# Kernel tuning notes

Hardware: AMD Instinct MI355X
Metric: run time of the kernel (lower is better)

The kernel has to match this reference:

```python
import jax, jax.numpy as jnp
import numpy as np

N_NODES = 50000


def _sage_conv(x, src, dst, Wl, bl, Wr):
    # mean-aggregate source features onto targets (PyG SAGEConv, aggr='mean')
    msg = x[src]                                             # [E, C_in] gather
    s = jax.ops.segment_sum(msg, dst, num_segments=N_NODES)  # [N, C_in]
    cnt = jax.ops.segment_sum(jnp.ones((src.shape[0],), x.dtype), dst,
                              num_segments=N_NODES)          # [N]
    agg = s / jnp.maximum(cnt, 1.0)[:, None]
    # out = lin_l(agg) + lin_r(x); bias only on lin_l
    return agg @ Wl.T + bl + x @ Wr.T


def setup_inputs() -> dict:
    key = jax.random.key(0)
    ks = jax.random.split(key, 8)
    in_c, hid_c, out_c = 128, 128, 64
    n_edges = 800000
    x = jax.random.normal(ks[0], (N_NODES, in_c), dtype=jnp.float32)
    edge_index = jax.random.randint(ks[1], (2, n_edges), 0, N_NODES, dtype=jnp.int64)
    sc = lambda k, shp: jax.random.normal(k, shp, dtype=jnp.float32) / np.sqrt(shp[1])
    return {
        "x": x,
        "edge_index": edge_index,
        "W1l": sc(ks[2], (hid_c, in_c)),
        "b1l": jnp.zeros((hid_c,), jnp.float32),
        "W1r": sc(ks[3], (hid_c, in_c)),
        "W2l": sc(ks[4], (out_c, hid_c)),
        "b2l": jnp.zeros((out_c,), jnp.float32),
        "W2r": sc(ks[5], (out_c, hid_c)),
    }


def reference(x, edge_index, W1l, b1l, W1r, W2l, b2l, W2r):
    src, dst = edge_index[0], edge_index[1]
    h = jax.nn.relu(_sage_conv(x, src, dst, W1l, b1l, W1r))
    # dropout(p=0.5) is identity at inference (training=False)
    return _sage_conv(h, src, dst, W2l, b2l, W2r)
```

## Files before the change

kernel.cpp:

```cpp
#include <hip/hip_runtime.h>
#include <hip/hip_bf16.h>

#define N_NODES 50000
#define N_EDGES 800000
#define N_BUCKETS 196
#define BUCKET_CAP 8192
#define POISON 0xAAAAAAAAu

#define XCVT_BLK 6250
#define WCVT_BLK 48
#define EPB 2048
#define BKT_BLK 391

typedef __attribute__((ext_vector_type(8))) short short8;
typedef __attribute__((ext_vector_type(4))) float floatx4;

static __device__ __forceinline__ float bf16_lo(unsigned int v) {
  union { unsigned int u; float f; } c; c.u = v << 16; return c.f;
}
static __device__ __forceinline__ float bf16_hi(unsigned int v) {
  union { unsigned int u; float f; } c; c.u = v & 0xffff0000u; return c.f;
}
static __device__ __forceinline__ unsigned short f32_to_bf16_rne(float f) {
  union { float f; unsigned int u; } c; c.f = f;
  unsigned int u = c.u;
  unsigned int r = (u + 0x7fffu + ((u >> 16) & 1u)) >> 16;
  return (unsigned short)r;
}
static __device__ __forceinline__ unsigned int pack2(float a, float b) {
  return (unsigned int)f32_to_bf16_rne(a) | ((unsigned int)f32_to_bf16_rne(b) << 16);
}
static __device__ __forceinline__ uint2 pack4(float4 v) {
  return (uint2){pack2(v.x, v.y), pack2(v.z, v.w)};
}
static __device__ __forceinline__ void accum8(float* acc, uint4 v) {
  acc[0] += bf16_lo(v.x); acc[1] += bf16_hi(v.x);
  acc[2] += bf16_lo(v.y); acc[3] += bf16_hi(v.y);
  acc[4] += bf16_lo(v.z); acc[5] += bf16_hi(v.z);
  acc[6] += bf16_lo(v.w); acc[7] += bf16_hi(v.w);
}

__global__ __launch_bounds__(256) void prep_bucket_kernel(
    const float4* __restrict__ x4, uint2* __restrict__ xb4,
    const float4* __restrict__ w1l4, const float4* __restrict__ w1r4,
    const float4* __restrict__ w2l4, const float4* __restrict__ w2r4,
    uint2* __restrict__ o1l, uint2* __restrict__ o1r,
    uint2* __restrict__ o2l, uint2* __restrict__ o2r,
    const int* __restrict__ src, const int* __restrict__ dst,
    unsigned int* __restrict__ bcur, unsigned int* __restrict__ ebuf) {
  __shared__ int hist[N_BUCKETS];
  __shared__ int base[N_BUCKETS];
  const int b = blockIdx.x, tid = threadIdx.x;
  if (b < XCVT_BLK) {
    int i = b * 256 + tid;
    xb4[i] = pack4(x4[i]);
    return;
  }
  if (b < XCVT_BLK + WCVT_BLK) {
    int j = (b - XCVT_BLK) * 256 + tid;
    const float4* in; uint2* out; int o2, NJ;
    if (j < 4096)       { in = w1l4; out = o1l; o2 = j;         NJ = 128; }
    else if (j < 8192)  { in = w1r4; out = o1r; o2 = j - 4096;  NJ = 128; }
    else if (j < 10240) { in = w2l4; out = o2l; o2 = j - 8192;  NJ = 64; }
    else                { in = w2r4; out = o2r; o2 = j - 10240; NJ = 64; }
    int half = o2 & 1;
    int rest = o2 >> 1;
    int col  = rest % NJ;
    int qk   = rest / NJ;
    int quad = qk & 3, kb = qk >> 2;
    out[o2] = pack4(in[col * 32 + kb * 8 + quad * 2 + half]);
    return;
  }
  const int eb = b - XCVT_BLK - WCVT_BLK;
  for (int i = tid; i < N_BUCKETS; i += 256) hist[i] = 0;
  __syncthreads();
  const int e0 = eb * EPB;
  int bk[8], rk[8];
  unsigned int pk[8];
  bool val[8];
  #pragma unroll
  for (int k = 0; k < 8; ++k) {
    int e = e0 + k * 256 + tid;
    val[k] = (e < N_EDGES);
    if (val[k]) {
      int d = dst[e], s = src[e];
      bk[k] = d >> 8;
      pk[k] = ((unsigned int)(d & 255) << 16) | (unsigned int)s;
      rk[k] = atomicAdd(&hist[bk[k]], 1);
    }
  }
  __syncthreads();
  for (int i = tid; i < N_BUCKETS; i += 256) {
    int h = hist[i];
    base[i] = h ? (int)(atomicAdd(&bcur[i], (unsigned int)h) - POISON) : 0;
  }
  __syncthreads();
  #pragma unroll
  for (int k = 0; k < 8; ++k) {
    if (val[k]) {
      unsigned int p = (unsigned int)(base[bk[k]] + rk[k]);
      if (p < BUCKET_CAP) ebuf[(size_t)bk[k] * BUCKET_CAP + p] = pk[k];
    }
  }
}

__global__ __launch_bounds__(256) void local_csr_kernel(
    const unsigned int* __restrict__ ebuf, const unsigned int* __restrict__ bcur,
    int* __restrict__ start_g, int* __restrict__ cnt_g, int* __restrict__ eidx) {
  const int b = blockIdx.x;
  int nb = (int)(bcur[b] - POISON);
  nb = max(0, min(nb, BUCKET_CAP));
  __shared__ int cnt[256];
  __shared__ int loff[256];
  __shared__ int ws[4];
  cnt[threadIdx.x] = 0;
  __syncthreads();
  const unsigned int* eb = ebuf + (size_t)b * BUCKET_CAP;
  for (int i = threadIdx.x; i < nb; i += 256)
    atomicAdd(&cnt[eb[i] >> 16], 1);
  __syncthreads();
  const int lane = threadIdx.x & 63, wid = threadIdx.x >> 6;
  int v = cnt[threadIdx.x];
  int incl = v;
  #pragma unroll
  for (int d = 1; d < 64; d <<= 1) {
    int t = __shfl_up(incl, d, 64);
    if (lane >= d) incl += t;
  }
  if (lane == 63) ws[wid] = incl;
  __syncthreads();
  int add = 0;
  #pragma unroll
  for (int w = 0; w < 4; ++w) if (w < wid) add += ws[w];
  int excl = add + incl - v;
  loff[threadIdx.x] = excl;
  int node = b * 256 + threadIdx.x;
  if (node < N_NODES) {
    start_g[node] = b * BUCKET_CAP + excl;
    cnt_g[node] = v;
  }
  __syncthreads();
  for (int i = threadIdx.x; i < nb; i += 256) {
    unsigned int p = eb[i];
    int pos = atomicAdd(&loff[p >> 16], 1);
    eidx[(size_t)b * BUCKET_CAP + pos] = (int)(p & 0xffffu);
  }
}

__global__ __launch_bounds__(256) void agg_kernel(
    const uint4* __restrict__ in,
    const int* __restrict__ start_g, const int* __restrict__ cnt_g,
    const int* __restrict__ eidx, uint4* __restrict__ out) {
  const int lane = threadIdx.x & 63;
  const int sub = lane >> 4;
  const int l16 = lane & 15;
  int node = blockIdx.x * 4 + (threadIdx.x >> 6);
  if (node >= N_NODES) return;
  int e0 = start_g[node];
  int c = cnt_g[node];
  int e1 = e0 + c;

  float acc[8];
  #pragma unroll
  for (int t = 0; t < 8; ++t) acc[t] = 0.f;

  int e = e0;
  for (; e + 16 <= e1; e += 16) {
    int s0 = eidx[e + sub];
    int s1 = eidx[e + 4 + sub];
    int s2 = eidx[e + 8 + sub];
    int s3 = eidx[e + 12 + sub];
    uint4 v0 = in[(size_t)s0 * 16 + l16];
    uint4 v1 = in[(size_t)s1 * 16 + l16];
    uint4 v2 = in[(size_t)s2 * 16 + l16];
    uint4 v3 = in[(size_t)s3 * 16 + l16];
    accum8(acc, v0); accum8(acc, v1); accum8(acc, v2); accum8(acc, v3);
  }
  for (; e + 8 <= e1; e += 8) {
    int s0 = eidx[e + sub];
    int s1 = eidx[e + 4 + sub];
    uint4 v0 = in[(size_t)s0 * 16 + l16];
    uint4 v1 = in[(size_t)s1 * 16 + l16];
    accum8(acc, v0); accum8(acc, v1);
  }
  for (; e < e1; e += 4) {
    int ee = e + sub;
    if (ee < e1) accum8(acc, in[(size_t)eidx[ee] * 16 + l16]);
  }
  #pragma unroll
  for (int d = 16; d < 64; d <<= 1) {
    #pragma unroll
    for (int t = 0; t < 8; ++t) acc[t] += __shfl_xor(acc[t], d, 64);
  }
  if (sub == 0) {
    float inv = 1.0f / fmaxf((float)c, 1.0f);
    uint4 o;
    o.x = pack2(acc[0] * inv, acc[1] * inv);
    o.y = pack2(acc[2] * inv, acc[3] * inv);
    o.z = pack2(acc[4] * inv, acc[5] * inv);
    o.w = pack2(acc[6] * inv, acc[7] * inv);
    out[(size_t)node * 16 + l16] = o;
  }
}

__global__ __launch_bounds__(256) void fused_gemm_kernel(
    const uint4* __restrict__ aggb4, const uint4* __restrict__ xb4,
    const unsigned short* __restrict__ W1l, const unsigned short* __restrict__ W1r,
    const float* __restrict__ b1,
    const unsigned short* __restrict__ W2l, const unsigned short* __restrict__ W2r,
    const float* __restrict__ b2,
    unsigned short* __restrict__ z, unsigned short* __restrict__ rbuf) {
  __shared__ unsigned short lds_a[64 * 136];
  __shared__ unsigned short lds_x[64 * 136];
  const int tid = threadIdx.x, lane = tid & 63, wave = tid >> 6;
  const int quad = lane >> 4, r16 = lane & 15;
  const int cg = wave & 1, tw = wave >> 1;
  const int col0 = cg * 64;
  const int n0 = blockIdx.x * 64;

  #pragma unroll
  for (int k = 0; k < 4; ++k) {
    int idx = k * 256 + tid;
    int row = idx >> 4, col = idx & 15;
    int gr = n0 + row; if (gr >= N_NODES) gr = N_NODES - 1;
    ((uint4*)lds_a)[row * 17 + col] = aggb4[(size_t)gr * 16 + col];
    ((uint4*)lds_x)[row * 17 + col] = xb4[(size_t)gr * 16 + col];
  }
  __syncthreads();

  const unsigned short* As[2] = {lds_a, lds_x};
  const unsigned short* Ws[2] = {W1l, W1r};
  floatx4 acc1[2][4] = {};
  #pragma unroll
  for (int rt = 0; rt < 2; ++rt) {
    int lrow = tw * 32 + rt * 16;
    #pragma unroll
    for (int s = 0; s < 2; ++s) {
      const unsigned short* Ar = As[s] + (lrow + r16) * 136 + quad * 8;
      #pragma unroll
      for (int kb = 0; kb < 4; ++kb) {
        short8 a = *(const short8*)(Ar + kb * 32);
        const unsigned short* Wf = Ws[s] + ((size_t)(kb * 4 + quad) * 128) * 8;
        #pragma unroll
        for (int c = 0; c < 4; ++c) {
          short8 bfr = *(const short8*)(Wf + (size_t)(col0 + c * 16 + r16) * 8);
          acc1[rt][c] = __builtin_amdgcn_mfma_f32_16x16x32_bf16(a, bfr, acc1[rt][c], 0, 0, 0);
        }
      }
    }
  }
  __syncthreads();

  #pragma unroll
  for (int rt = 0; rt < 2; ++rt) {
    int lrow0 = tw * 32 + rt * 16 + quad * 4;
    #pragma unroll
    for (int c = 0; c < 4; ++c) {
      int j = col0 + c * 16 + r16;
      float bv = b1[j];
      #pragma unroll
      for (int r = 0; r < 4; ++r)
        lds_a[(lrow0 + r) * 136 + j] = f32_to_bf16_rne(fmaxf(acc1[rt][c][r] + bv, 0.f));
    }
  }
  __syncthreads();

  const unsigned short* W = cg ? W2r : W2l;
  unsigned short* outp = cg ? rbuf : z;
  #pragma unroll
  for (int rt = 0; rt < 2; ++rt) {
    int lrow = tw * 32 + rt * 16;
    floatx4 acc[4] = {};
    const unsigned short* la = lds_a + (lrow + r16) * 136 + quad * 8;
    #pragma unroll
    for (int kb = 0; kb < 4; ++kb) {
      short8 a = *(const short8*)(la + kb * 32);
      const unsigned short* Wf = W + ((size_t)(kb * 4 + quad) * 64) * 8;
      #pragma unroll
      for (int c = 0; c < 4; ++c) {
        short8 bfr = *(const short8*)(Wf + (size_t)(c * 16 + r16) * 8);
        acc[c] = __builtin_amdgcn_mfma_f32_16x16x32_bf16(a, bfr, acc[c], 0, 0, 0);
      }
    }
    int orow0 = n0 + lrow + quad * 4;
    #pragma unroll
    for (int c = 0; c < 4; ++c) {
      int j = c * 16 + r16;
      float bv = cg ? b2[j] : 0.f;
      #pragma unroll
      for (int r = 0; r < 4; ++r) {
        int node = orow0 + r;
        if (node < N_NODES)
          outp[(size_t)node * 64 + j] = f32_to_bf16_rne(acc[c][r] + bv);
      }
    }
  }
}

__global__ __launch_bounds__(256) void final_agg_kernel(
    const uint4* __restrict__ z4, const uint4* __restrict__ r4,
    const int* __restrict__ start_g, const int* __restrict__ cnt_g,
    const int* __restrict__ eidx, float* __restrict__ outp) {
  const int lane = threadIdx.x & 63;
  const int sub = lane >> 3;
  const int l8 = lane & 7;
  int node = blockIdx.x * 4 + (threadIdx.x >> 6);
  if (node >= N_NODES) return;
  int e0 = start_g[node];
  int c = cnt_g[node];
  int e1 = e0 + c;

  float acc[8];
  #pragma unroll
  for (int t = 0; t < 8; ++t) acc[t] = 0.f;

  int e = e0;
  for (; e + 16 <= e1; e += 16) {
    int s0 = eidx[e + sub];
    int s1 = eidx[e + 8 + sub];
    uint4 v0 = z4[(size_t)s0 * 8 + l8];
    uint4 v1 = z4[(size_t)s1 * 8 + l8];
    accum8(acc, v0);
    accum8(acc, v1);
  }
  for (; e < e1; e += 8) {
    int ee = e + sub;
    if (ee < e1) accum8(acc, z4[(size_t)eidx[ee] * 8 + l8]);
  }
  #pragma unroll
  for (int d = 8; d < 64; d <<= 1) {
    #pragma unroll
    for (int t = 0; t < 8; ++t) acc[t] += __shfl_xor(acc[t], d, 64);
  }
  if (sub == 0) {
    float inv = 1.0f / fmaxf((float)c, 1.0f);
    uint4 rv = r4[(size_t)node * 8 + l8];
    float4* op = (float4*)(outp + (size_t)node * 64 + l8 * 8);
    float4 a, b;
    a.x = acc[0] * inv + bf16_lo(rv.x); a.y = acc[1] * inv + bf16_hi(rv.x);
    a.z = acc[2] * inv + bf16_lo(rv.y); a.w = acc[3] * inv + bf16_hi(rv.y);
    b.x = acc[4] * inv + bf16_lo(rv.z); b.y = acc[5] * inv + bf16_hi(rv.z);
    b.z = acc[6] * inv + bf16_lo(rv.w); b.w = acc[7] * inv + bf16_hi(rv.w);
    op[0] = a; op[1] = b;
  }
}

extern "C" void kernel_launch(void* const* d_in, const int* in_sizes, int n_in,
                              void* d_out, int out_size, void* d_ws, size_t ws_size,
                              hipStream_t stream) {
  (void)in_sizes; (void)n_in; (void)out_size; (void)ws_size;
  const float* x   = (const float*)d_in[0];
  const int*   ei  = (const int*)d_in[1];
  const float* W1l = (const float*)d_in[2];
  const float* b1l = (const float*)d_in[3];
  const float* W1r = (const float*)d_in[4];
  const float* W2l = (const float*)d_in[5];
  const float* b2l = (const float*)d_in[6];
  const float* W2r = (const float*)d_in[7];
  const int* src = ei;
  const int* dst = ei + N_EDGES;

  char* ws = (char*)d_ws;
  size_t p = 0;
  auto alloc = [&](size_t bytes) {
    char* q = ws + p;
    p = (p + bytes + 255) & ~(size_t)255;
    return q;
  };
  unsigned int* bcur = (unsigned int*)alloc((size_t)N_BUCKETS * 4);
  int* start_g = (int*)alloc((size_t)N_NODES * 4);
  int* cnt_g   = (int*)alloc((size_t)N_NODES * 4);
  unsigned int* ebuf = (unsigned int*)alloc((size_t)N_BUCKETS * BUCKET_CAP * 4);
  int* eidx    = (int*)alloc((size_t)N_BUCKETS * BUCKET_CAP * 4);
  unsigned short* xb   = (unsigned short*)alloc((size_t)N_NODES * 128 * 2);
  unsigned short* aggb = (unsigned short*)alloc((size_t)N_NODES * 128 * 2);
  unsigned short* zb   = (unsigned short*)alloc((size_t)N_NODES * 64 * 2);
  unsigned short* rb   = (unsigned short*)alloc((size_t)N_NODES * 64 * 2);
  unsigned short* w1lb = (unsigned short*)alloc(128 * 128 * 2);
  unsigned short* w1rb = (unsigned short*)alloc(128 * 128 * 2);
  unsigned short* w2lb = (unsigned short*)alloc(64 * 128 * 2);
  unsigned short* w2rb = (unsigned short*)alloc(64 * 128 * 2);

  prep_bucket_kernel<<<XCVT_BLK + WCVT_BLK + BKT_BLK, 256, 0, stream>>>(
      (const float4*)x, (uint2*)xb,
      (const float4*)W1l, (const float4*)W1r, (const float4*)W2l, (const float4*)W2r,
      (uint2*)w1lb, (uint2*)w1rb, (uint2*)w2lb, (uint2*)w2rb,
      src, dst, bcur, (unsigned int*)ebuf);
  local_csr_kernel<<<N_BUCKETS, 256, 0, stream>>>(
      (const unsigned int*)ebuf, bcur, start_g, cnt_g, eidx);
  agg_kernel<<<(N_NODES + 3) / 4, 256, 0, stream>>>(
      (const uint4*)xb, start_g, cnt_g, eidx, (uint4*)aggb);
  fused_gemm_kernel<<<(N_NODES + 63) / 64, 256, 0, stream>>>(
      (const uint4*)aggb, (const uint4*)xb, w1lb, w1rb, b1l, w2lb, w2rb, b2l, zb, rb);
  final_agg_kernel<<<(N_NODES + 3) / 4, 256, 0, stream>>>(
      (const uint4*)zb, (const uint4*)rb, start_g, cnt_g, eidx, (float*)d_out);
}
```

Baseline: 189.5 us.

## Map one small lane group per node in aggregation kernels and widen CSR block

Both aggregation kernels now give each node a 16-lane (or 8-lane) group instead of a full wave. Each group walks its edges serially with 8 gathers in flight per step, so the cross-lane shuffle reduction and the idle-lane masking on the final write go away, and more nodes share each wave. The local CSR build runs 512 threads per bucket, with only the first 256 doing the scan. The trade-off is less edge-level parallelism per node, so high-degree nodes may become a longer serial tail. The first aggregation kernel also drops its node bounds check, which is only safe because the node count divides evenly by 16.

```diff
diff --git a/kernel.cpp b/kernel.cpp
--- a/kernel.cpp
+++ b/kernel.cpp
@@ -104,7 +104,7 @@
   }
 }
 
-__global__ __launch_bounds__(256) void local_csr_kernel(
+__global__ __launch_bounds__(512) void local_csr_kernel(
     const unsigned int* __restrict__ ebuf, const unsigned int* __restrict__ bcur,
     int* __restrict__ start_g, int* __restrict__ cnt_g, int* __restrict__ eidx) {
   const int b = blockIdx.x;
@@ -113,34 +113,37 @@
   __shared__ int cnt[256];
   __shared__ int loff[256];
   __shared__ int ws[4];
-  cnt[threadIdx.x] = 0;
+  if (threadIdx.x < 256) cnt[threadIdx.x] = 0;
   __syncthreads();
   const unsigned int* eb = ebuf + (size_t)b * BUCKET_CAP;
-  for (int i = threadIdx.x; i < nb; i += 256)
+  for (int i = threadIdx.x; i < nb; i += 512)
     atomicAdd(&cnt[eb[i] >> 16], 1);
   __syncthreads();
-  const int lane = threadIdx.x & 63, wid = threadIdx.x >> 6;
-  int v = cnt[threadIdx.x];
+  const int t256 = threadIdx.x & 255;
+  const int lane = threadIdx.x & 63, wid = (threadIdx.x >> 6) & 3;
+  int v = cnt[t256];
   int incl = v;
   #pragma unroll
   for (int d = 1; d < 64; d <<= 1) {
     int t = __shfl_up(incl, d, 64);
     if (lane >= d) incl += t;
   }
-  if (lane == 63) ws[wid] = incl;
+  if (threadIdx.x < 256 && lane == 63) ws[wid] = incl;
   __syncthreads();
   int add = 0;
   #pragma unroll
   for (int w = 0; w < 4; ++w) if (w < wid) add += ws[w];
   int excl = add + incl - v;
-  loff[threadIdx.x] = excl;
-  int node = b * 256 + threadIdx.x;
-  if (node < N_NODES) {
-    start_g[node] = b * BUCKET_CAP + excl;
-    cnt_g[node] = v;
-  }
-  __syncthreads();
-  for (int i = threadIdx.x; i < nb; i += 256) {
+  if (threadIdx.x < 256) {
+    loff[t256] = excl;
+    int node = b * 256 + t256;
+    if (node < N_NODES) {
+      start_g[node] = b * BUCKET_CAP + excl;
+      cnt_g[node] = v;
+    }
+  }
+  __syncthreads();
+  for (int i = threadIdx.x; i < nb; i += 512) {
     unsigned int p = eb[i];
     int pos = atomicAdd(&loff[p >> 16], 1);
     eidx[(size_t)b * BUCKET_CAP + pos] = (int)(p & 0xffffu);
@@ -151,11 +154,8 @@
     const uint4* __restrict__ in,
     const int* __restrict__ start_g, const int* __restrict__ cnt_g,
     const int* __restrict__ eidx, uint4* __restrict__ out) {
-  const int lane = threadIdx.x & 63;
-  const int sub = lane >> 4;
-  const int l16 = lane & 15;
-  int node = blockIdx.x * 4 + (threadIdx.x >> 6);
-  if (node >= N_NODES) return;
+  const int l16 = threadIdx.x & 15;
+  const int node = blockIdx.x * 16 + (threadIdx.x >> 4);
   int e0 = start_g[node];
   int c = cnt_g[node];
   int e1 = e0 + c;
@@ -165,42 +165,37 @@
   for (int t = 0; t < 8; ++t) acc[t] = 0.f;
 
   int e = e0;
-  for (; e + 16 <= e1; e += 16) {
-    int s0 = eidx[e + sub];
-    int s1 = eidx[e + 4 + sub];
-    int s2 = eidx[e + 8 + sub];
-    int s3 = eidx[e + 12 + sub];
-    uint4 v0 = in[(size_t)s0 * 16 + l16];
-    uint4 v1 = in[(size_t)s1 * 16 + l16];
-    uint4 v2 = in[(size_t)s2 * 16 + l16];
-    uint4 v3 = in[(size_t)s3 * 16 + l16];
-    accum8(acc, v0); accum8(acc, v1); accum8(acc, v2); accum8(acc, v3);
-  }
   for (; e + 8 <= e1; e += 8) {
-    int s0 = eidx[e + sub];
-    int s1 = eidx[e + 4 + sub];
-    uint4 v0 = in[(size_t)s0 * 16 + l16];
-    uint4 v1 = in[(size_t)s1 * 16 + l16];
-    accum8(acc, v0); accum8(acc, v1);
-  }
-  for (; e < e1; e += 4) {
-    int ee = e + sub;
-    if (ee < e1) accum8(acc, in[(size_t)eidx[ee] * 16 + l16]);
-  }
-  #pragma unroll
-  for (int d = 16; d < 64; d <<= 1) {
-    #pragma unroll
-    for (int t = 0; t < 8; ++t) acc[t] += __shfl_xor(acc[t], d, 64);
-  }
-  if (sub == 0) {
-    float inv = 1.0f / fmaxf((float)c, 1.0f);
-    uint4 o;
-    o.x = pack2(acc[0] * inv, acc[1] * inv);
-    o.y = pack2(acc[2] * inv, acc[3] * inv);
-    o.z = pack2(acc[4] * inv, acc[5] * inv);
-    o.w = pack2(acc[6] * inv, acc[7] * inv);
-    out[(size_t)node * 16 + l16] = o;
-  }
+    int s[8];
+    #pragma unroll
+    for (int k = 0; k < 8; ++k) s[k] = eidx[e + k];
+    uint4 v[8];
+    #pragma unroll
+    for (int k = 0; k < 8; ++k) v[k] = in[(size_t)s[k] * 16 + l16];
+    #pragma unroll
+    for (int k = 0; k < 8; ++k) accum8(acc, v[k]);
+  }
+  if (e + 4 <= e1) {
+    int s[4];
+    #pragma unroll
+    for (int k = 0; k < 4; ++k) s[k] = eidx[e + k];
+    uint4 v[4];
+    #pragma unroll
+    for (int k = 0; k < 4; ++k) v[k] = in[(size_t)s[k] * 16 + l16];
+    #pragma unroll
+    for (int k = 0; k < 4; ++k) accum8(acc, v[k]);
+    e += 4;
+  }
+  for (; e < e1; ++e)
+    accum8(acc, in[(size_t)eidx[e] * 16 + l16]);
+
+  float inv = 1.0f / fmaxf((float)c, 1.0f);
+  uint4 o;
+  o.x = pack2(acc[0] * inv, acc[1] * inv);
+  o.y = pack2(acc[2] * inv, acc[3] * inv);
+  o.z = pack2(acc[4] * inv, acc[5] * inv);
+  o.w = pack2(acc[6] * inv, acc[7] * inv);
+  out[(size_t)node * 16 + l16] = o;
 }
 
 __global__ __launch_bounds__(256) void fused_gemm_kernel(
@@ -301,10 +296,8 @@
     const uint4* __restrict__ z4, const uint4* __restrict__ r4,
     const int* __restrict__ start_g, const int* __restrict__ cnt_g,
     const int* __restrict__ eidx, float* __restrict__ outp) {
-  const int lane = threadIdx.x & 63;
-  const int sub = lane >> 3;
-  const int l8 = lane & 7;
-  int node = blockIdx.x * 4 + (threadIdx.x >> 6);
+  const int l8 = threadIdx.x & 7;
+  const int node = blockIdx.x * 32 + (threadIdx.x >> 3);
   if (node >= N_NODES) return;
   int e0 = start_g[node];
   int c = cnt_g[node];
@@ -315,34 +308,39 @@
   for (int t = 0; t < 8; ++t) acc[t] = 0.f;
 
   int e = e0;
-  for (; e + 16 <= e1; e += 16) {
-    int s0 = eidx[e + sub];
-    int s1 = eidx[e + 8 + sub];
-    uint4 v0 = z4[(size_t)s0 * 8 + l8];
-    uint4 v1 = z4[(size_t)s1 * 8 + l8];
-    accum8(acc, v0);
-    accum8(acc, v1);
-  }
-  for (; e < e1; e += 8) {
-    int ee = e + sub;
-    if (ee < e1) accum8(acc, z4[(size_t)eidx[ee] * 8 + l8]);
-  }
-  #pragma unroll
-  for (int d = 8; d < 64; d <<= 1) {
-    #pragma unroll
-    for (int t = 0; t < 8; ++t) acc[t] += __shfl_xor(acc[t], d, 64);
-  }
-  if (sub == 0) {
-    float inv = 1.0f / fmaxf((float)c, 1.0f);
-    uint4 rv = r4[(size_t)node * 8 + l8];
-    float4* op = (float4*)(outp + (size_t)node * 64 + l8 * 8);
-    float4 a, b;
-    a.x = acc[0] * inv + bf16_lo(rv.x); a.y = acc[1] * inv + bf16_hi(rv.x);
-    a.z = acc[2] * inv + bf16_lo(rv.y); a.w = acc[3] * inv + bf16_hi(rv.y);
-    b.x = acc[4] * inv + bf16_lo(rv.z); b.y = acc[5] * inv + bf16_hi(rv.z);
-    b.z = acc[6] * inv + bf16_lo(rv.w); b.w = acc[7] * inv + bf16_hi(rv.w);
-    op[0] = a; op[1] = b;
-  }
+  for (; e + 8 <= e1; e += 8) {
+    int s[8];
+    #pragma unroll
+    for (int k = 0; k < 8; ++k) s[k] = eidx[e + k];
+    uint4 v[8];
+    #pragma unroll
+    for (int k = 0; k < 8; ++k) v[k] = z4[(size_t)s[k] * 8 + l8];
+    #pragma unroll
+    for (int k = 0; k < 8; ++k) accum8(acc, v[k]);
+  }
+  if (e + 4 <= e1) {
+    int s[4];
+    #pragma unroll
+    for (int k = 0; k < 4; ++k) s[k] = eidx[e + k];
+    uint4 v[4];
+    #pragma unroll
+    for (int k = 0; k < 4; ++k) v[k] = z4[(size_t)s[k] * 8 + l8];
+    #pragma unroll
+    for (int k = 0; k < 4; ++k) accum8(acc, v[k]);
+    e += 4;
+  }
+  for (; e < e1; ++e)
+    accum8(acc, z4[(size_t)eidx[e] * 8 + l8]);
+
+  float inv = 1.0f / fmaxf((float)c, 1.0f);
+  uint4 rv = r4[(size_t)node * 8 + l8];
+  float4* op = (float4*)(outp + (size_t)node * 64 + l8 * 8);
+  float4 a, b;
+  a.x = acc[0] * inv + bf16_lo(rv.x); a.y = acc[1] * inv + bf16_hi(rv.x);
+  a.z = acc[2] * inv + bf16_lo(rv.y); a.w = acc[3] * inv + bf16_hi(rv.y);
+  b.x = acc[4] * inv + bf16_lo(rv.z); b.y = acc[5] * inv + bf16_hi(rv.z);
+  b.z = acc[6] * inv + bf16_lo(rv.w); b.w = acc[7] * inv + bf16_hi(rv.w);
+  op[0] = a; op[1] = b;
 }
 
 extern "C" void kernel_launch(void* const* d_in, const int* in_sizes, int n_in,
@@ -386,12 +384,12 @@
       (const float4*)W1l, (const float4*)W1r, (const float4*)W2l, (const float4*)W2r,
       (uint2*)w1lb, (uint2*)w1rb, (uint2*)w2lb, (uint2*)w2rb,
       src, dst, bcur, (unsigned int*)ebuf);
-  local_csr_kernel<<<N_BUCKETS, 256, 0, stream>>>(
+  local_csr_kernel<<<N_BUCKETS, 512, 0, stream>>>(
       (const unsigned int*)ebuf, bcur, start_g, cnt_g, eidx);
-  agg_kernel<<<(N_NODES + 3) / 4, 256, 0, stream>>>(
+  agg_kernel<<<(N_NODES + 15) / 16, 256, 0, stream>>>(
       (const uint4*)xb, start_g, cnt_g, eidx, (uint4*)aggb);
   fused_gemm_kernel<<<(N_NODES + 63) / 64, 256, 0, stream>>>(
       (const uint4*)aggb, (const uint4*)xb, w1lb, w1rb, b1l, w2lb, w2rb, b2l, zb, rb);
-  final_agg_kernel<<<(N_NODES + 3) / 4, 256, 0, stream>>>(
+  final_agg_kernel<<<(N_NODES + 31) / 32, 256, 0, stream>>>(
       (const uint4*)zb, (const uint4*)rb, start_g, cnt_g, eidx, (float*)d_out);
 }
```

Result: faster. 181.4 us (-4.3%).
